# Performance work log

Measured on AMD Instinct MI355X. Metric: run time of the kernel, lower is better.

The kernel has to match this reference:

```python
import jax, jax.numpy as jnp
import numpy as np

B, S, HID = 2, 2048, 1024
NH, HD = 4, 256
SCALE = HD ** -0.5


def _rope(x, fr, fi):
    # x: [B,S,NH,HD]; fr/fi: [S,HD//2]
    b, s, n, d = x.shape
    xr = x.reshape(b, s, n, d // 2, 2)
    re, im = xr[..., 0], xr[..., 1]
    fr = fr[None, :, None, :]
    fi = fi[None, :, None, :]
    rr = re * fr - im * fi
    ri = re * fi + im * fr
    return jnp.stack((rr, ri), axis=-1).reshape(b, s, n, d)


def setup_inputs() -> dict:
    key = jax.random.key(0)
    k1, k2, k3 = jax.random.split(key, 3)
    hidden_states = jax.random.normal(k1, (B, S, HID), dtype=jnp.float32)
    # RoPE frequencies (standard theta=10000)
    inv_freq = 1.0 / (10000.0 ** (np.arange(0, HD, 2, dtype=np.float32) / HD))  # [HD//2]
    t = np.arange(S, dtype=np.float32)
    ang = np.outer(t, inv_freq)  # [S, HD//2]
    freqs_real = jnp.asarray(np.cos(ang), dtype=jnp.float32)
    freqs_imag = jnp.asarray(np.sin(ang), dtype=jnp.float32)
    # causal additive mask [1,1,S,S]
    causal = jnp.tril(jnp.ones((S, S), dtype=bool))
    mask = jnp.where(causal, 0.0, -1e9).astype(jnp.float32)[None, None]
    W_qkv = jax.random.normal(k2, (3 * HID, HID), dtype=jnp.float32) * (HID ** -0.5)
    W_o = jax.random.normal(k3, (HID, HID), dtype=jnp.float32) * (HID ** -0.5)
    return {"hidden_states": hidden_states, "freqs_real": freqs_real,
            "freqs_imag": freqs_imag, "mask": mask, "W_qkv": W_qkv, "W_o": W_o}


def reference(hidden_states, freqs_real, freqs_imag, mask, W_qkv, W_o):
    b, s, _ = hidden_states.shape
    qkv = hidden_states @ W_qkv.T  # [B,S,3*HID]
    qkv = qkv.reshape(b, s, 3, NH, HD)
    q, k, v = qkv[:, :, 0], qkv[:, :, 1], qkv[:, :, 2]
    q = _rope(q, freqs_real, freqs_imag)
    k = _rope(k, freqs_real, freqs_imag)
    scores = jnp.einsum('bqhd,bkhd->bhqk', q * SCALE, k) + mask  # [B,NH,S,S]
    probs = jax.nn.softmax(scores, axis=-1)
    attn = jnp.einsum('bhqk,bkhd->bqhd', probs, v).reshape(b, s, HID)
    return attn @ W_o.T
```

## Files before the change

### kernel.cpp

```cpp
#include <hip/hip_runtime.h>
#include <stdint.h>

#define NB 2
#define NS 2048
#define NHID 1024
#define NHEADS 4
#define DHEAD 256
#define NP 128
#define QK_SCALE 0.0625f

typedef unsigned short ushort_t;
typedef __bf16 bf16x8 __attribute__((ext_vector_type(8)));
typedef float floatx4 __attribute__((ext_vector_type(4)));
typedef short shortx8 __attribute__((ext_vector_type(8)));
typedef unsigned short ushortx4 __attribute__((ext_vector_type(4)));
typedef unsigned short ushortx8 __attribute__((ext_vector_type(8)));

__device__ __forceinline__ float bf2f(ushort_t u) {
    unsigned int x = ((unsigned int)u) << 16;
    return __builtin_bit_cast(float, x);
}
__device__ __forceinline__ ushort_t f2bf(float f) {
    unsigned int u = __builtin_bit_cast(unsigned int, f);
    u += 0x7fff + ((u >> 16) & 1);
    return (ushort_t)(u >> 16);
}

__device__ __forceinline__ floatx4 mfma16(bf16x8 a, bf16x8 b, floatx4 c) {
    return __builtin_amdgcn_mfma_f32_16x16x32_bf16(a, b, c, 0, 0, 0);
}

__device__ __forceinline__ void gload_lds16(const void* g, void* l) {
    __builtin_amdgcn_global_load_lds(
        (const __attribute__((address_space(1))) void*)g,
        (__attribute__((address_space(3))) void*)l, 16, 0, 0);
}

#define N4_H (4096 * 1024 / 4)
#define N4_WQ (3072 * 1024 / 4)
#define N4_WO (1024 * 1024 / 4)
__global__ __launch_bounds__(256) void cast3_kernel(const float* __restrict__ inH,
                                                    const float* __restrict__ inWq,
                                                    const float* __restrict__ inWo,
                                                    ushort_t* __restrict__ out) {
    int i = blockIdx.x * 256 + threadIdx.x;
    const float* src;
    int j = i;
    if (i < N4_H) {
        src = inH;
    } else if (i < N4_H + N4_WQ) {
        src = inWq; j = i - N4_H;
    } else {
        src = inWo; j = i - (N4_H + N4_WQ);
    }
    float4 v = ((const float4*)src)[j];
    ushortx4 o = { f2bf(v.x), f2bf(v.y), f2bf(v.z), f2bf(v.w) };
    ((ushortx4*)out)[i] = o;
}

__global__ __launch_bounds__(256) void gemm_bt_f32s(const ushort_t* __restrict__ A,
                                                    const ushort_t* __restrict__ Bt,
                                                    float* __restrict__ C0,
                                                    float* __restrict__ C1,
                                                    int M, int N, int K) {
    __shared__ ushort_t sA[4][128 * 32];
    __shared__ ushort_t sB[4][128 * 32];
    const int t = threadIdx.x;
    const int f = blockIdx.x;
    const int xcd = f & 7;
    const int idx = f >> 3;
    const int im = idx >> 4;
    const int in = (idx >> 1) & 7;
    const int kz = idx & 1;
    const int m0 = (xcd * 4 + im) * 128;
    const int n0 = in * 128;
    float* Cout = kz ? C1 : C0;
    const int kbeg = kz * (K / 2);
    const int w = t >> 6, l = t & 63;
    const int wm = (w >> 1) * 64, wn = (w & 1) * 64;
    const int lc = l & 15, lq = l >> 4;

    floatx4 acc[4][4];
#pragma unroll
    for (int i = 0; i < 4; i++)
#pragma unroll
        for (int j = 0; j < 4; j++) acc[i][j] = (floatx4){0.f, 0.f, 0.f, 0.f};

    const int srow = w * 16 + (l >> 2);
    const int scol = (((l & 3) - (l >> 2) - (l >> 4)) & 3) * 8;
    const ushort_t* Ag = A + (size_t)(m0 + srow) * K + scol + kbeg;
    const ushort_t* Bg = Bt + (size_t)(n0 + srow) * K + scol + kbeg;
    const int lofs = t * 8;

    auto stage = [&](int bsel, int kk) {
        ushort_t* lA = &sA[bsel][lofs];
        ushort_t* lB = &sB[bsel][lofs];
        gload_lds16(Ag + kk, lA);
        gload_lds16(Ag + kk + (size_t)64 * K, lA + 2048);
        gload_lds16(Bg + kk, lB);
        gload_lds16(Bg + kk + (size_t)64 * K, lB + 2048);
    };
    auto compute = [&](int bsel) {
        const ushort_t* cA = sA[bsel];
        const ushort_t* cB = sB[bsel];
        bf16x8 af[4], bfv[4];
#pragma unroll
        for (int i = 0; i < 4; i++) {
            int R = wm + i * 16 + lc;
            af[i] = *(const bf16x8*)&cA[R * 32 + ((lq + R + (R >> 2)) & 3) * 8];
        }
#pragma unroll
        for (int j = 0; j < 4; j++) {
            int R = wn + j * 16 + lc;
            bfv[j] = *(const bf16x8*)&cB[R * 32 + ((lq + R + (R >> 2)) & 3) * 8];
        }
#pragma unroll
        for (int i = 0; i < 4; i++)
#pragma unroll
            for (int j = 0; j < 4; j++)
                acc[i][j] = mfma16(af[i], bfv[j], acc[i][j]);
    };

    stage(0, 0); stage(1, 32); stage(2, 64);
#pragma unroll 1
    for (int s = 0; s <= 16 - 4; ++s) {
        asm volatile("s_waitcnt vmcnt(8)" ::: "memory");
        __builtin_amdgcn_sched_barrier(0);
        __builtin_amdgcn_s_barrier();
        asm volatile("" ::: "memory");
        compute(s & 3);
        stage((s + 3) & 3, (s + 3) * 32);
    }
    asm volatile("s_waitcnt vmcnt(8)" ::: "memory");
    __builtin_amdgcn_sched_barrier(0);
    __builtin_amdgcn_s_barrier();
    asm volatile("" ::: "memory");
    compute(13 & 3);
    asm volatile("s_waitcnt vmcnt(4)" ::: "memory");
    __builtin_amdgcn_sched_barrier(0);
    __builtin_amdgcn_s_barrier();
    asm volatile("" ::: "memory");
    compute(14 & 3);
    asm volatile("s_waitcnt vmcnt(0)" ::: "memory");
    __builtin_amdgcn_sched_barrier(0);
    __builtin_amdgcn_s_barrier();
    asm volatile("" ::: "memory");
    compute(15 & 3);

#pragma unroll
    for (int i = 0; i < 4; i++) {
        int row = m0 + wm + i * 16 + lq * 4;
#pragma unroll
        for (int j = 0; j < 4; j++) {
            int col = n0 + wn + j * 16 + lc;
#pragma unroll
            for (int r = 0; r < 4; r++)
                Cout[(size_t)(row + r) * N + col] = acc[i][j][r];
        }
    }
}

__global__ __launch_bounds__(256) void add_f32(const float* __restrict__ a,
                                               const float* __restrict__ b,
                                               float* __restrict__ o, int n4) {
    int i = blockIdx.x * 256 + threadIdx.x;
    if (i < n4) {
        float4 x = ((const float4*)a)[i];
        float4 y = ((const float4*)b)[i];
        float4 z = { x.x + y.x, x.y + y.y, x.z + y.z, x.w + y.w };
        ((float4*)o)[i] = z;
    }
}

__global__ __launch_bounds__(512, 2) void gemm_qkv(const ushort_t* __restrict__ A,
                                                   const ushort_t* __restrict__ Bt,
                                                   const float* __restrict__ fre,
                                                   const float* __restrict__ fim,
                                                   ushort_t* __restrict__ Q,
                                                   ushort_t* __restrict__ Kk,
                                                   ushort_t* __restrict__ Vt) {
    __shared__ ushort_t sA[4][8192];
    __shared__ ushort_t sB[4][8192];
    const int t = threadIdx.x;
    const int f = blockIdx.x;
    const int xcd = f & 7;
    const int idx = f >> 3;
    const int mreg = xcd >> 1, nreg = xcd & 1;
    const int im = idx & 3, in = idx >> 2;
    const int m0 = (mreg * 4 + im) * 256;
    const int n0 = (nreg * 6 + in) * 256;
    const int w = t >> 6, l = t & 63;
    const int wr = w >> 2, wc = w & 3;
    const int wrm = wr * 128, wcn = wc * 64;
    const int lc = l & 15, lq = l >> 4;

    floatx4 acc[8][4];
#pragma unroll
    for (int i = 0; i < 8; i++)
#pragma unroll
        for (int j = 0; j < 4; j++) acc[i][j] = (floatx4){0.f, 0.f, 0.f, 0.f};

    const int srow = t >> 2;
    const int sc8 = ((((t & 3) - (t >> 2) - (t >> 4)) & 3)) * 8;
    const ushort_t* Ab = A + (size_t)(m0 + srow) * 1024 + sc8;
    const ushort_t* Bb = Bt + (size_t)(n0 + srow) * 1024 + sc8;
    const int ldst = t * 8;

    auto STAGE = [&](int buf, int kk) {
        gload_lds16(Ab + kk, &sA[buf][ldst]);
        gload_lds16(Ab + (size_t)128 * 1024 + kk, &sA[buf][4096 + ldst]);
        gload_lds16(Bb + kk, &sB[buf][ldst]);
        gload_lds16(Bb + (size_t)128 * 1024 + kk, &sB[buf][4096 + ldst]);
    };
    auto COMPUTE = [&](int buf) {
        const ushort_t* cA = sA[buf];
        const ushort_t* cB = sB[buf];
        bf16x8 af[8], bfr[4];
#pragma unroll
        for (int i = 0; i < 8; i++) {
            const int R = wrm + i * 16 + lc;
            af[i] = *(const bf16x8*)&cA[R * 32 + ((lq + R + (R >> 2)) & 3) * 8];
        }
#pragma unroll
        for (int j = 0; j < 4; j++) {
            const int R = wcn + j * 16 + lc;
            bfr[j] = *(const bf16x8*)&cB[R * 32 + ((lq + R + (R >> 2)) & 3) * 8];
        }
        asm volatile("s_waitcnt lgkmcnt(0)" ::: "memory");
        __builtin_amdgcn_sched_barrier(0);
        __builtin_amdgcn_s_setprio(1);
#pragma unroll
        for (int i = 0; i < 8; i++)
#pragma unroll
            for (int j = 0; j < 4; j++)
                acc[i][j] = mfma16(af[i], bfr[j], acc[i][j]);
        __builtin_amdgcn_s_setprio(0);
    };

#define QWAITV(n) do { asm volatile("s_waitcnt vmcnt(" #n ")" ::: "memory"); \
                       __builtin_amdgcn_sched_barrier(0); } while (0)
#define QBAR      do { asm volatile("" ::: "memory"); \
                       __builtin_amdgcn_s_barrier(); \
                       asm volatile("" ::: "memory"); } while (0)

    STAGE(0, 0); STAGE(1, 32); STAGE(2, 64);

#pragma unroll 1
    for (int kt = 0; kt < 29; ++kt) {
        QWAITV(8);
        QBAR;
        STAGE((kt + 3) & 3, (kt + 3) * 32);
        COMPUTE(kt & 3);
    }
    QWAITV(8); QBAR; COMPUTE(29 & 3);
    QWAITV(4); QBAR; COMPUTE(30 & 3);
    QWAITV(0); QBAR; COMPUTE(31 & 3);

    const int sect = n0 >> 10;
#pragma unroll
    for (int i = 0; i < 8; i++) {
        int row = m0 + wrm + i * 16 + lq * 4;
        int bb = row >> 11;
        int srow2 = row & 2047;
#pragma unroll
        for (int j = 0; j < 4; j++) {
            int col = n0 + wcn + j * 16 + lc;
            int d = col & 255;
            int h = (col >> 8) & 3;
            int bh = bb * NHEADS + h;
            if (sect == 2) {
                ushortx4 pack = { f2bf(acc[i][j][0]), f2bf(acc[i][j][1]),
                                  f2bf(acc[i][j][2]), f2bf(acc[i][j][3]) };
                *(ushortx4*)&Vt[((size_t)bh * 256 + d) * NS + srow2] = pack;
            } else {
                int p = d >> 1;
                int odd = d & 1;
                ushort_t* dst = (sect == 0) ? Q : Kk;
#pragma unroll
                for (int r = 0; r < 4; r++) {
                    float v = acc[i][j][r];
                    float vp = __shfl_xor(v, 1);
                    int s = srow2 + r;
                    float c = fre[s * NP + p], si = fim[s * NP + p];
                    float out = odd ? (vp * si + v * c) : (v * c - vp * si);
                    if (sect == 0) out *= QK_SCALE;
                    dst[((size_t)bh * NS + s) * DHEAD + d] = f2bf(out);
                }
            }
        }
    }
}

#define BQ3 128
#define BKV3 64
#define PPAD 72
#define CHCAP 6
#define NPART_BH 51
#define OPART_SPLIT 224

__global__ __launch_bounds__(256, 2) void flash_attn4(const ushort_t* __restrict__ Q,
                                                      const ushort_t* __restrict__ K,
                                                      const ushort_t* __restrict__ Vt,
                                                      ushort_t* __restrict__ OpA,
                                                      ushort_t* __restrict__ OpB,
                                                      float* __restrict__ ml) {
    __shared__ ushort_t sK[BKV3 * 256];
    __shared__ ushort_t sV[DHEAD * 64];
    __shared__ ushort_t sP[4][16 * PPAD];

    int rem = blockIdx.x, qt = 15, nsp;
    for (;;) {
        nsp = (2 * (qt + 1) + CHCAP - 1) / CHCAP;
        if (rem < nsp) break;
        rem -= nsp;
        qt--;
    }
    const int nch = 2 * (qt + 1);
    const int cbeg = rem * CHCAP;
    const int cend = (cbeg + CHCAP < nch) ? cbeg + CHCAP : nch;

    const int h = blockIdx.y, b = blockIdx.z;
    const int t = threadIdx.x, w = t >> 6, l = t & 63;
    const int lc = l & 15, lq = l >> 4;
    const int bh = b * NHEADS + h;
    const size_t base = (size_t)bh * NS * DHEAD;
    const int q0 = qt * BQ3;

    const int krb = w * 2 + (l >> 5);
    const int kck = ((l & 31) - (krb & 7)) & 31;
    const size_t koff = (size_t)krb * 256 + kck * 8;
    const int vrb = w * 8 + (l >> 3);
    const int vck = ((l & 7) - (vrb & 7)) & 7;
    const size_t voff = (size_t)vrb * NS + vck * 8;
    ushort_t* dK = &sK[w * 512 + l * 8];
    ushort_t* dV = &sV[w * 512 + l * 8];

    bf16x8 qf[2][8];
#pragma unroll
    for (int gq = 0; gq < 2; gq++) {
        const ushort_t* qrow = Q + base + (size_t)(q0 + w * 32 + gq * 16 + lc) * DHEAD + lq * 8;
#pragma unroll
        for (int dk = 0; dk < 8; dk++) qf[gq][dk] = *(const bf16x8*)(qrow + dk * 32);
    }

    floatx4 accO[2][16];
#pragma unroll
    for (int gq = 0; gq < 2; gq++)
#pragma unroll
        for (int j = 0; j < 16; j++) accO[gq][j] = (floatx4){0.f, 0.f, 0.f, 0.f};
    float lrun[2][4] = {{0.f, 0.f, 0.f, 0.f}, {0.f, 0.f, 0.f, 0.f}};

    for (int kc = cbeg; kc < cend; kc++) {
        const int kb = kc * BKV3;
        __syncthreads();
        {
            const ushort_t* ksrc = K + base + (size_t)kb * 256 + koff;
            const ushort_t* vsrc = Vt + base + kb + voff;
#pragma unroll
            for (int j = 0; j < 8; j++)
                gload_lds16(ksrc + j * (8 * 256), dK + j * 2048);
#pragma unroll
            for (int j = 0; j < 8; j++)
                gload_lds16(vsrc + j * (32 * NS), dV + j * 2048);
        }
        __syncthreads();

        floatx4 sfr[2][4];
#pragma unroll
        for (int gq = 0; gq < 2; gq++)
#pragma unroll
            for (int g = 0; g < 4; g++) sfr[gq][g] = (floatx4){0.f, 0.f, 0.f, 0.f};
#pragma unroll
        for (int dk = 0; dk < 8; dk++) {
#pragma unroll
            for (int g = 0; g < 4; g++) {
                int R = g * 16 + lc;
                int phys = (dk * 4 + lq + (R & 7)) & 31;
                bf16x8 bk = *(const bf16x8*)&sK[R * 256 + phys * 8];
                sfr[0][g] = mfma16(qf[0][dk], bk, sfr[0][g]);
                sfr[1][g] = mfma16(qf[1][dk], bk, sfr[1][g]);
            }
        }

        if (kc >= nch - 2) {
#pragma unroll
            for (int gq = 0; gq < 2; gq++)
#pragma unroll
                for (int g = 0; g < 4; g++) {
                    int kg = kb + g * 16 + lc;
                    int qr = q0 + w * 32 + gq * 16 + lq * 4;
#pragma unroll
                    for (int r = 0; r < 4; r++)
                        if (kg > qr + r) sfr[gq][g][r] = -1e30f;
                }
        }

        ushort_t* pw = sP[w];
#pragma unroll
        for (int gq = 0; gq < 2; gq++) {
#pragma unroll
            for (int g = 0; g < 4; g++)
#pragma unroll
                for (int r = 0; r < 4; r++) {
                    float p = __expf(sfr[gq][g][r]);
                    lrun[gq][r] += p;
                    pw[(lq * 4 + r) * PPAD + g * 16 + lc] = f2bf(p);
                }
            bf16x8 ap0 = *(const bf16x8*)&pw[lc * PPAD + lq * 8];
            bf16x8 ap1 = *(const bf16x8*)&pw[lc * PPAD + 32 + lq * 8];
#pragma unroll
            for (int j = 0; j < 16; j++) {
                int D = j * 16 + lc;
                int ph0 = (lq + (D & 7)) & 7;
                int ph1 = (4 + lq + (D & 7)) & 7;
                bf16x8 bv0 = *(const bf16x8*)&sV[D * 64 + ph0 * 8];
                bf16x8 bv1 = *(const bf16x8*)&sV[D * 64 + ph1 * 8];
                accO[gq][j] = mfma16(ap0, bv0, accO[gq][j]);
                accO[gq][j] = mfma16(ap1, bv1, accO[gq][j]);
            }
        }
    }

    const int pid = bh * NPART_BH + blockIdx.x;
    ushort_t* op = (pid < OPART_SPLIT) ? OpA + (size_t)pid * (128 * 256)
                                       : OpB + (size_t)(pid - OPART_SPLIT) * (128 * 256);
#pragma unroll
    for (int gq = 0; gq < 2; gq++) {
#pragma unroll
        for (int r = 0; r < 4; r++) {
            int row = w * 32 + gq * 16 + lq * 4 + r;
#pragma unroll
            for (int j = 0; j < 16; j++)
                op[row * 256 + j * 16 + lc] = f2bf(accO[gq][j][r]);
            float lv = lrun[gq][r];
#pragma unroll
            for (int off = 1; off < 16; off <<= 1) lv += __shfl_xor(lv, off);
            if (lc == 0) ml[(size_t)pid * 128 + row] = lv;
        }
    }
}

__global__ __launch_bounds__(256) void combine_parts2(const ushort_t* __restrict__ OpA,
                                                      const ushort_t* __restrict__ OpB,
                                                      const float* __restrict__ ml,
                                                      ushort_t* __restrict__ O) {
    const int qt = blockIdx.x >> 3, rsub = blockIdx.x & 7;
    const int h = blockIdx.y, b = blockIdx.z;
    const int bh = b * NHEADS + h;
    int bbase = 0;
    for (int q = 15; q > qt; q--) bbase += (2 * (q + 1) + CHCAP - 1) / CHCAP;
    const int nsp = (2 * (qt + 1) + CHCAP - 1) / CHCAP;
    const int pid0 = bh * NPART_BH + bbase;

    const int t = threadIdx.x;
    const int rl = t >> 4;
    const int c0 = (t & 15) * 16;
    const int row = rsub * 16 + rl;

    float so[16];
#pragma unroll
    for (int k = 0; k < 16; k++) so[k] = 0.f;
    float sl = 0.f;

    for (int i = 0; i < nsp; i++) {
        int pid = pid0 + i;
        const ushort_t* op = (pid < OPART_SPLIT)
                                 ? OpA + (size_t)pid * (128 * 256)
                                 : OpB + (size_t)(pid - OPART_SPLIT) * (128 * 256);
        const ushort_t* p = op + row * 256 + c0;
        ushortx8 a0 = *(const ushortx8*)p;
        ushortx8 a1 = *(const ushortx8*)(p + 8);
#pragma unroll
        for (int k = 0; k < 8; k++) {
            so[k] += bf2f(a0[k]);
            so[8 + k] += bf2f(a1[k]);
        }
        sl += ml[(size_t)pid * 128 + row];
    }

    float inv = 1.f / sl;
    ushortx8 o0, o1;
#pragma unroll
    for (int k = 0; k < 8; k++) {
        o0[k] = f2bf(so[k] * inv);
        o1[k] = f2bf(so[8 + k] * inv);
    }
    int s = qt * BQ3 + row;
    ushort_t* dst = O + ((size_t)(b * NS + s) * NHEADS + h) * DHEAD + c0;
    *(ushortx8*)dst = o0;
    *(ushortx8*)(dst + 8) = o1;
}

extern "C" void kernel_launch(void* const* d_in, const int* in_sizes, int n_in,
                              void* d_out, int out_size, void* d_ws, size_t ws_size,
                              hipStream_t stream) {
    const float* hidden = (const float*)d_in[0];
    const float* fre = (const float*)d_in[1];
    const float* fim = (const float*)d_in[2];
    const float* Wqkv = (const float*)d_in[4];
    const float* Wo = (const float*)d_in[5];

    char* ws = (char*)d_ws;
    ushort_t* hb    = (ushort_t*)(ws);
    ushort_t* wqkvb = (ushort_t*)(ws + 8388608);
    ushort_t* wob   = (ushort_t*)(ws + 14680064);
    ushort_t* qb    = (ushort_t*)(ws + 16777216);
    ushort_t* kb    = (ushort_t*)(ws + 25165824);
    ushort_t* vtb   = (ushort_t*)(ws + 33554432);
    ushort_t* OpA   = (ushort_t*)(ws);
    ushort_t* OpB   = (ushort_t*)(ws + 41943040);
    ushort_t* oattn = (ushort_t*)(ws + 16777216);
    float*    gP0   = (float*)(ws + 25165824);
    float*    gP1   = (float*)(ws + 41943040);
    float*    ml    = (float*)(ws + 58720256);

    cast3_kernel<<<(N4_H + N4_WQ + N4_WO) / 256, 256, 0, stream>>>(hidden, Wqkv, Wo, hb);

    gemm_qkv<<<dim3(192), 512, 0, stream>>>(
        hb, wqkvb, fre, fim, qb, kb, vtb);

    flash_attn4<<<dim3(NPART_BH, NHEADS, NB), 256, 0, stream>>>(qb, kb, vtb, OpA, OpB, ml);
    combine_parts2<<<dim3(128, NHEADS, NB), 256, 0, stream>>>(OpA, OpB, ml, oattn);

    gemm_bt_f32s<<<dim3(512), 256, 0, stream>>>(
        oattn, wob, gP0, gP1, 4096, 1024, 1024);
    add_f32<<<4096, 256, 0, stream>>>(gP0, gP1, (float*)d_out, 4096 * 1024 / 4);
}
```

Before: 217.2 us.

## Retile QKV GEMM to 256x192 tiles with K=64 double-buffered interleaved pipeline

The QKV projection GEMM moves from 256x256 output tiles (192 blocks) to 256x192 tiles (256 blocks), so all 256 CUs on the device get one block. The K step grows from 32 to 64 with a two-stage buffer instead of four, and a new 8-way swizzle is used. Each iteration is split into four MFMA phases, and the next tile's A and B loads are issued between them. The RoPE epilogue now derives section and head per 16-column fragment, because a tile can span section boundaries. The cost is more barriers per iteration and shallower prefetch depth, which may expose more memory latency.

```diff
diff --git a/kernel.cpp b/kernel.cpp
--- a/kernel.cpp
+++ b/kernel.cpp
@@ -179,8 +179,8 @@
                                                    ushort_t* __restrict__ Q,
                                                    ushort_t* __restrict__ Kk,
                                                    ushort_t* __restrict__ Vt) {
-    __shared__ ushort_t sA[4][8192];
-    __shared__ ushort_t sB[4][8192];
+    __shared__ ushort_t sA[2][16384];
+    __shared__ ushort_t sB[2][12288];
     const int t = threadIdx.x;
     const int f = blockIdx.x;
     const int xcd = f & 7;
@@ -188,85 +188,141 @@
     const int mreg = xcd >> 1, nreg = xcd & 1;
     const int im = idx & 3, in = idx >> 2;
     const int m0 = (mreg * 4 + im) * 256;
-    const int n0 = (nreg * 6 + in) * 256;
+    const int n0 = (nreg * 8 + in) * 192;
     const int w = t >> 6, l = t & 63;
     const int wr = w >> 2, wc = w & 3;
-    const int wrm = wr * 128, wcn = wc * 64;
+    const int wrm = wr * 128, wcn = wc * 48;
     const int lc = l & 15, lq = l >> 4;
 
-    floatx4 acc[8][4];
+    floatx4 acc[8][3];
 #pragma unroll
     for (int i = 0; i < 8; i++)
 #pragma unroll
-        for (int j = 0; j < 4; j++) acc[i][j] = (floatx4){0.f, 0.f, 0.f, 0.f};
-
-    const int srow = t >> 2;
-    const int sc8 = ((((t & 3) - (t >> 2) - (t >> 4)) & 3)) * 8;
-    const ushort_t* Ab = A + (size_t)(m0 + srow) * 1024 + sc8;
-    const ushort_t* Bb = Bt + (size_t)(n0 + srow) * 1024 + sc8;
+        for (int j = 0; j < 3; j++) acc[i][j] = (floatx4){0.f, 0.f, 0.f, 0.f};
+
+    const int arow = t >> 3;
+    const int ac8 = ((((t & 7) - (arow & 7)) & 7)) * 8;
+    const ushort_t* Ab = A + (size_t)(m0 + arow) * 1024 + ac8;
+    const ushort_t* Bb = Bt + (size_t)(n0 + arow) * 1024 + ac8;
     const int ldst = t * 8;
 
-    auto STAGE = [&](int buf, int kk) {
-        gload_lds16(Ab + kk, &sA[buf][ldst]);
-        gload_lds16(Ab + (size_t)128 * 1024 + kk, &sA[buf][4096 + ldst]);
+    auto STAGE_A2 = [&](int buf, int half, int kk) {
+        gload_lds16(Ab + (size_t)(half * 128) * 1024 + kk, &sA[buf][half * 8192 + ldst]);
+        gload_lds16(Ab + (size_t)(half * 128 + 64) * 1024 + kk, &sA[buf][half * 8192 + 4096 + ldst]);
+    };
+    auto STAGE_B3 = [&](int buf, int kk) {
         gload_lds16(Bb + kk, &sB[buf][ldst]);
-        gload_lds16(Bb + (size_t)128 * 1024 + kk, &sB[buf][4096 + ldst]);
+        gload_lds16(Bb + (size_t)64 * 1024 + kk, &sB[buf][4096 + ldst]);
+        gload_lds16(Bb + (size_t)128 * 1024 + kk, &sB[buf][8192 + ldst]);
     };
-    auto COMPUTE = [&](int buf) {
-        const ushort_t* cA = sA[buf];
-        const ushort_t* cB = sB[buf];
-        bf16x8 af[8], bfr[4];
-#pragma unroll
-        for (int i = 0; i < 8; i++) {
-            const int R = wrm + i * 16 + lc;
-            af[i] = *(const bf16x8*)&cA[R * 32 + ((lq + R + (R >> 2)) & 3) * 8];
-        }
-#pragma unroll
-        for (int j = 0; j < 4; j++) {
-            const int R = wcn + j * 16 + lc;
-            bfr[j] = *(const bf16x8*)&cB[R * 32 + ((lq + R + (R >> 2)) & 3) * 8];
-        }
-        asm volatile("s_waitcnt lgkmcnt(0)" ::: "memory");
-        __builtin_amdgcn_sched_barrier(0);
+
+#define QWAITV0  do { asm volatile("s_waitcnt vmcnt(0)" ::: "memory"); \
+                      __builtin_amdgcn_sched_barrier(0); } while (0)
+#define QWAITL   do { asm volatile("s_waitcnt lgkmcnt(0)" ::: "memory"); \
+                      __builtin_amdgcn_sched_barrier(0); } while (0)
+#define QBAR     do { asm volatile("" ::: "memory"); \
+                      __builtin_amdgcn_s_barrier(); \
+                      asm volatile("" ::: "memory"); } while (0)
+
+    STAGE_A2(0, 0, 0); STAGE_A2(0, 1, 0); STAGE_B3(0, 0);
+
+#pragma unroll 1
+    for (int kt = 0; kt < 16; ++kt) {
+        const int b = kt & 1, nb = b ^ 1;
+        const int kn = (kt + 1) * 64;
+        const ushort_t* cA = sA[b];
+        const ushort_t* cB = sB[b];
+        bf16x8 af[4][2], bfr[3][2];
+
+        QWAITV0;
+        QBAR;
+#pragma unroll
+        for (int ii = 0; ii < 4; ii++) {
+            const int R = wrm + ii * 16 + lc;
+            af[ii][0] = *(const bf16x8*)&cA[R * 64 + ((lq + R) & 7) * 8];
+            af[ii][1] = *(const bf16x8*)&cA[R * 64 + ((4 + lq + R) & 7) * 8];
+        }
+#pragma unroll
+        for (int jj = 0; jj < 2; jj++) {
+            const int R = wcn + jj * 16 + lc;
+            bfr[jj][0] = *(const bf16x8*)&cB[R * 64 + ((lq + R) & 7) * 8];
+            bfr[jj][1] = *(const bf16x8*)&cB[R * 64 + ((4 + lq + R) & 7) * 8];
+        }
+        if (kt < 15) STAGE_A2(nb, 0, kn);
+        QWAITL;
         __builtin_amdgcn_s_setprio(1);
 #pragma unroll
-        for (int i = 0; i < 8; i++)
-#pragma unroll
-            for (int j = 0; j < 4; j++)
-                acc[i][j] = mfma16(af[i], bfr[j], acc[i][j]);
+        for (int ii = 0; ii < 4; ii++)
+#pragma unroll
+            for (int jj = 0; jj < 2; jj++) {
+                acc[ii][jj] = mfma16(af[ii][0], bfr[jj][0], acc[ii][jj]);
+                acc[ii][jj] = mfma16(af[ii][1], bfr[jj][1], acc[ii][jj]);
+            }
         __builtin_amdgcn_s_setprio(0);
-    };
-
-#define QWAITV(n) do { asm volatile("s_waitcnt vmcnt(" #n ")" ::: "memory"); \
-                       __builtin_amdgcn_sched_barrier(0); } while (0)
-#define QBAR      do { asm volatile("" ::: "memory"); \
-                       __builtin_amdgcn_s_barrier(); \
-                       asm volatile("" ::: "memory"); } while (0)
-
-    STAGE(0, 0); STAGE(1, 32); STAGE(2, 64);
-
-#pragma unroll 1
-    for (int kt = 0; kt < 29; ++kt) {
-        QWAITV(8);
+
         QBAR;
-        STAGE((kt + 3) & 3, (kt + 3) * 32);
-        COMPUTE(kt & 3);
-    }
-    QWAITV(8); QBAR; COMPUTE(29 & 3);
-    QWAITV(4); QBAR; COMPUTE(30 & 3);
-    QWAITV(0); QBAR; COMPUTE(31 & 3);
-
-    const int sect = n0 >> 10;
+        {
+            const int R = wcn + 32 + lc;
+            bfr[2][0] = *(const bf16x8*)&cB[R * 64 + ((lq + R) & 7) * 8];
+            bfr[2][1] = *(const bf16x8*)&cB[R * 64 + ((4 + lq + R) & 7) * 8];
+        }
+        if (kt < 15) STAGE_A2(nb, 1, kn);
+        QWAITL;
+        __builtin_amdgcn_s_setprio(1);
+#pragma unroll
+        for (int ii = 0; ii < 4; ii++) {
+            acc[ii][2] = mfma16(af[ii][0], bfr[2][0], acc[ii][2]);
+            acc[ii][2] = mfma16(af[ii][1], bfr[2][1], acc[ii][2]);
+        }
+        __builtin_amdgcn_s_setprio(0);
+
+        QBAR;
+#pragma unroll
+        for (int ii = 0; ii < 4; ii++) {
+            const int R = wrm + 64 + ii * 16 + lc;
+            af[ii][0] = *(const bf16x8*)&cA[R * 64 + ((lq + R) & 7) * 8];
+            af[ii][1] = *(const bf16x8*)&cA[R * 64 + ((4 + lq + R) & 7) * 8];
+        }
+        if (kt < 15) STAGE_B3(nb, kn);
+        QWAITL;
+        __builtin_amdgcn_s_setprio(1);
+#pragma unroll
+        for (int ii = 0; ii < 4; ii++) {
+            acc[4 + ii][2] = mfma16(af[ii][0], bfr[2][0], acc[4 + ii][2]);
+            acc[4 + ii][2] = mfma16(af[ii][1], bfr[2][1], acc[4 + ii][2]);
+        }
+        __builtin_amdgcn_s_setprio(0);
+
+        QBAR;
+#pragma unroll
+        for (int jj = 0; jj < 2; jj++) {
+            const int R = wcn + jj * 16 + lc;
+            bfr[jj][0] = *(const bf16x8*)&cB[R * 64 + ((lq + R) & 7) * 8];
+            bfr[jj][1] = *(const bf16x8*)&cB[R * 64 + ((4 + lq + R) & 7) * 8];
+        }
+        QWAITL;
+        __builtin_amdgcn_s_setprio(1);
+#pragma unroll
+        for (int ii = 0; ii < 4; ii++)
+#pragma unroll
+            for (int jj = 0; jj < 2; jj++) {
+                acc[4 + ii][jj] = mfma16(af[ii][0], bfr[jj][0], acc[4 + ii][jj]);
+                acc[4 + ii][jj] = mfma16(af[ii][1], bfr[jj][1], acc[4 + ii][jj]);
+            }
+        __builtin_amdgcn_s_setprio(0);
+    }
+
 #pragma unroll
     for (int i = 0; i < 8; i++) {
         int row = m0 + wrm + i * 16 + lq * 4;
         int bb = row >> 11;
         int srow2 = row & 2047;
 #pragma unroll
-        for (int j = 0; j < 4; j++) {
-            int col = n0 + wcn + j * 16 + lc;
-            int d = col & 255;
-            int h = (col >> 8) & 3;
+        for (int j = 0; j < 3; j++) {
+            int c0 = n0 + wcn + j * 16;
+            int sect = c0 >> 10;
+            int h = (c0 >> 8) & 3;
+            int d = (c0 & 255) + lc;
             int bh = bb * NHEADS + h;
             if (sect == 2) {
                 ushortx4 pack = { f2bf(acc[i][j][0]), f2bf(acc[i][j][1]),
@@ -516,7 +572,7 @@
 
     cast3_kernel<<<(N4_H + N4_WQ + N4_WO) / 256, 256, 0, stream>>>(hidden, Wqkv, Wo, hb);
 
-    gemm_qkv<<<dim3(192), 512, 0, stream>>>(
+    gemm_qkv<<<dim3(256), 512, 0, stream>>>(
         hb, wqkvb, fre, fim, qb, kb, vtb);
 
     flash_attn4<<<dim3(NPART_BH, NHEADS, NB), 256, 0, stream>>>(qb, kb, vtb, OpA, OpB, ml);
```

After: 200.5 us. -7.7%, faster.
